# Kernel tuning notes

Hardware: AMD Instinct MI355X
Metric: run time of the kernel (lower is better)

Reference implementation:

```python
import jax, jax.numpy as jnp
import numpy as np

EPS = 1e-6  # torch F.pairwise_distance default eps (added to diff before norm)


def setup_inputs() -> dict:
    key = jax.random.key(0)
    k1, k2 = jax.random.split(key)
    B, D, n = 4096, 1024, 64
    K = n * n
    x = jax.random.normal(k1, (B, D), dtype=jnp.float32)
    weight = jax.random.normal(k2, (D, K), dtype=jnp.float32)  # SOM codebook
    # locations = [(gx, gy) for gx in range(n) for gy in range(n)]
    gx, gy = jnp.meshgrid(jnp.arange(n), jnp.arange(n), indexing='ij')
    locations = jnp.stack([gx, gy], axis=-1).reshape(K, 2).astype(jnp.float32)
    return {"x": x, "weight": weight, "locations": locations}


def _pairwise_l2(x, weight):
    # torch: norm(x[:, :, None] - weight[None] + EPS, p=2, dim=1) -> [B, K]
    # Expanded algebraically to avoid the [B, D, K] intermediate:
    D = x.shape[1]
    x2 = jnp.sum(x * x, axis=1, keepdims=True)            # [B, 1]
    w2 = jnp.sum(weight * weight, axis=0, keepdims=True)  # [1, K]
    xw = x @ weight                                        # [B, K] GEMM
    sx = jnp.sum(x, axis=1, keepdims=True)                 # [B, 1]
    sw = jnp.sum(weight, axis=0, keepdims=True)            # [1, K]
    d2 = x2 - 2.0 * xw + w2 + 2.0 * EPS * (sx - sw) + D * EPS * EPS
    return jnp.sqrt(jnp.maximum(d2, 0.0))


def reference(x, weight, locations):
    B = x.shape[0]
    dists = _pairwise_l2(x, weight)                        # [B, K]
    losses = jnp.min(dists, axis=1, keepdims=True)         # [B, 1]
    bmu_indexes = jnp.argmin(dists, axis=1, keepdims=True)  # [B, 1] int
    bmu_locations = locations[bmu_indexes]                 # [B, 1, 2]
    loss = jnp.sum(losses) / B                             # scalar
    return bmu_locations, loss, bmu_indexes
```

## Files before the change

kernel.cpp:

```cpp
#include <hip/hip_runtime.h>

#define EPS 1e-6f

constexpr int Bn = 4096;
constexpr int Dn = 1024;
constexpr int Kn = 4096;

typedef __attribute__((ext_vector_type(4))) float f32x4;
typedef __attribute__((ext_vector_type(2))) long long ll2;

__device__ inline int pk_fp8_lo(float a, float b, int old) {
    return __builtin_amdgcn_cvt_pk_fp8_f32(a, b, old, false);
}
__device__ inline int pk_fp8_hi(float a, float b, int old) {
    return __builtin_amdgcn_cvt_pk_fp8_f32(a, b, old, true);
}

__device__ inline float packcand(float s, int k) {
    unsigned b = __float_as_uint(fmaxf(s, 0.5f));
    return __uint_as_float((b & 0xFFFFF000u) | (unsigned)k);
}

__global__ __launch_bounds__(256) void som_prep(
    const float* __restrict__ x, const float* __restrict__ w,
    unsigned char* __restrict__ xf8, float* __restrict__ rrow,
    float* __restrict__ wtf, unsigned char* __restrict__ wf8,
    float* __restrict__ cpart, unsigned* __restrict__ ticket) {
    __shared__ float t[64][65];
    __shared__ float cp[4][64];
    __shared__ float red[8];
    const int tid = threadIdx.x;
    const int bid = blockIdx.x;
    if (bid == 0 && tid == 32) *ticket = 0u;
    if (bid < 2048) {
        const int lane = tid & 63, wid = tid >> 6;
        size_t i = (size_t)bid * 256 + tid;
        const float4* p = (const float4*)x;
        float4 a = p[i * 2], b = p[i * 2 + 1];
        int lo = pk_fp8_lo(a.x, a.y, 0); lo = pk_fp8_hi(a.z, a.w, lo);
        int hi = pk_fp8_lo(b.x, b.y, 0); hi = pk_fp8_hi(b.z, b.w, hi);
        ((int2*)xf8)[i] = make_int2(lo, hi);
        float s2 = a.x*a.x + a.y*a.y + a.z*a.z + a.w*a.w
                 + b.x*b.x + b.y*b.y + b.z*b.z + b.w*b.w;
        float s1 = a.x + a.y + a.z + a.w + b.x + b.y + b.z + b.w;
        #pragma unroll
        for (int off = 1; off < 64; off <<= 1) {
            s2 += __shfl_xor(s2, off);
            s1 += __shfl_xor(s1, off);
        }
        if (lane == 0) { red[wid] = s2; red[4 + wid] = s1; }
        __syncthreads();
        if (tid == 0)
            rrow[bid * 2] = (red[0] + red[1])
                + 2.f * EPS * (red[4] + red[5]) + (float)Dn * EPS * EPS;
        if (tid == 128)
            rrow[bid * 2 + 1] = (red[2] + red[3])
                + 2.f * EPS * (red[6] + red[7]) + (float)Dn * EPS * EPS;
    } else {
        const int tb = bid - 2048;
        const int kb = tb & 63, db = tb >> 6;
        const int k0 = kb * 64, d0 = db * 64;
        const int tx = tid & 63, ty = tid >> 6;
        #pragma unroll
        for (int i = 0; i < 16; ++i) {
            int d = i * 4 + ty;
            t[d][tx] = w[(size_t)(d0 + d) * Kn + k0 + tx];
        }
        __syncthreads();
        #pragma unroll
        for (int i = 0; i < 16; ++i) {
            int kr = i * 4 + ty;
            float v = t[tx][kr];
            wtf[(size_t)(k0 + kr) * Dn + d0 + tx] = v;
            wf8[(size_t)(k0 + kr) * Dn + d0 + tx] =
                (unsigned char)(pk_fp8_lo(v, v, 0) & 0xFF);
        }
        float cs = 0.f;
        #pragma unroll
        for (int j = 0; j < 16; ++j) {
            float v = t[ty * 16 + j][tx];
            cs = fmaf(v, v - 2.f * EPS, cs);
        }
        cp[ty][tx] = cs;
        __syncthreads();
        if (ty == 0)
            cpart[(size_t)db * Kn + k0 + tx] = cp[0][tx] + cp[1][tx] + cp[2][tx] + cp[3][tx];
    }
}

__global__ __launch_bounds__(256, 3) void som_gemm_fp8(
    const unsigned char* __restrict__ xf8, const unsigned char* __restrict__ wf8,
    const float* __restrict__ cpart, float* __restrict__ pval) {
    __shared__ __align__(16) unsigned char As[128 * 144];
    __shared__ __align__(16) unsigned char Bs[128 * 144];
    const int tid = threadIdx.x;
    const int lane = tid & 63;
    const int wid = tid >> 6;
    const int wm = wid >> 1, wn = wid & 1;
    const int f = blockIdx.x;
    const int xcd = f & 7;
    const int ib = f >> 3;
    const int rb = xcd * 4 + (ib & 3);
    const int cb = ib >> 2;
    const int rowBase = rb * 128, colBase = cb * 128;

    int offA[4];
    const unsigned char* gsrcA[4];
    const unsigned char* gsrcB[4];
    #pragma unroll
    for (int i = 0; i < 4; ++i) {
        int g = i * 256 + tid;
        int r = g >> 3, s = g & 7;
        offA[i] = r * 144 + (2 * (s & 1)) * 32 + (s >> 1) * 8;
        gsrcA[i] = xf8 + (size_t)(rowBase + r) * Dn + s * 16;
        gsrcB[i] = wf8 + (size_t)(colBase + r) * Dn + s * 16;
    }

    f32x4 acc[4][4] = {};
    ll2 ra[4], rbv[4];
    #pragma unroll
    for (int i = 0; i < 4; ++i) {
        ra[i]  = *(const ll2*)(gsrcA[i]);
        rbv[i] = *(const ll2*)(gsrcB[i]);
    }

    const int mrA = (wm * 64 + (lane & 15)) * 144;
    const int nrB = (wn * 64 + (lane & 15)) * 144;
    const int qoff = (lane >> 4) * 32;

    for (int it = 0; it < 8; ++it) {
        #pragma unroll
        for (int i = 0; i < 4; ++i) {
            *(long long*)&As[offA[i]]      = ra[i][0];
            *(long long*)&As[offA[i] + 32] = ra[i][1];
            *(long long*)&Bs[offA[i]]      = rbv[i][0];
            *(long long*)&Bs[offA[i] + 32] = rbv[i][1];
        }
        __syncthreads();
        if (it < 7) {
            int d0 = (it + 1) * 128;
            #pragma unroll
            for (int i = 0; i < 4; ++i) {
                ra[i]  = *(const ll2*)(gsrcA[i] + d0);
                rbv[i] = *(const ll2*)(gsrcB[i] + d0);
            }
        }
        #pragma unroll
        for (int kk2 = 0; kk2 < 2; ++kk2) {
            ll2 a2[4], b2[4];
            #pragma unroll
            for (int i = 0; i < 4; ++i) {
                a2[i] = *(const ll2*)&As[mrA + i * 16 * 144 + qoff + kk2 * 16];
                b2[i] = *(const ll2*)&Bs[nrB + i * 16 * 144 + qoff + kk2 * 16];
            }
            #pragma unroll
            for (int i = 0; i < 4; ++i)
                #pragma unroll
                for (int j = 0; j < 4; ++j) {
                    acc[i][j] = __builtin_amdgcn_mfma_f32_16x16x32_fp8_fp8(
                        a2[i][0], b2[j][0], acc[i][j], 0, 0, 0);
                    acc[i][j] = __builtin_amdgcn_mfma_f32_16x16x32_fp8_fp8(
                        a2[i][1], b2[j][1], acc[i][j], 0, 0, 0);
                }
        }
        __syncthreads();
    }

    const int cn = lane & 15, q = lane >> 4;
    const int nbase = colBase + wn * 64;
    float cv[4];
    #pragma unroll
    for (int j = 0; j < 4; ++j) {
        float s = 0.f;
        #pragma unroll
        for (int db = 0; db < 16; ++db)
            s += cpart[(size_t)db * Kn + nbase + j * 16 + cn];
        cv[j] = s;
    }
    #pragma unroll
    for (int i = 0; i < 4; ++i) {
        #pragma unroll
        for (int rg = 0; rg < 4; ++rg) {
            float p1 = 3.4e38f, p2 = 3.4e38f;
            #pragma unroll
            for (int j = 0; j < 4; ++j) {
                float p = packcand(fmaf(-2.f, acc[i][j][rg], cv[j]),
                                   nbase + j * 16 + cn);
                float lo = fminf(p1, p), hi = fmaxf(p1, p);
                p1 = lo; p2 = fminf(p2, hi);
            }
            #pragma unroll
            for (int off = 1; off < 16; off <<= 1) {
                float o1 = __shfl_xor(p1, off);
                float o2 = __shfl_xor(p2, off);
                float lo = fminf(p1, o1), hi = fmaxf(p1, o1);
                p1 = lo; p2 = fminf(hi, fminf(p2, o2));
            }
            if (cn == 0) {
                int mrow = rowBase + wm * 64 + i * 16 + q * 4 + rg;
                size_t e = (size_t)mrow * 128 + cb * 4 + wn * 2;
                pval[e] = p1; pval[e + 1] = p2;
            }
        }
    }
}

__global__ __launch_bounds__(256) void som_finalize(
    const float* __restrict__ x, const float* __restrict__ wtf,
    const float* __restrict__ cpart, const float* __restrict__ loc,
    const float* __restrict__ pval, const float* __restrict__ rrow,
    float* __restrict__ dist, float* __restrict__ out,
    unsigned* __restrict__ ticket) {
    __shared__ unsigned short lists[4][128];
    __shared__ float red2[4];
    __shared__ int finflag;
    const int tid = threadIdx.x;
    const int wv = tid >> 6, lane = tid & 63;
    const int row = blockIdx.x * 4 + wv;

    const float4* xr = (const float4*)(x + (size_t)row * Dn);
    float4 xv[4];
    #pragma unroll
    for (int j = 0; j < 4; ++j) xv[j] = xr[lane * 4 + j];
    const float rrv = rrow[row];

    float v0 = pval[(size_t)row * 128 + lane];
    float v1 = pval[(size_t)row * 128 + 64 + lane];
    float g = fminf(v0, v1);
    #pragma unroll
    for (int off = 1; off < 64; off <<= 1) g = fminf(g, __shfl_xor(g, off));
    const float thr = g + 30.0f;
    const unsigned long long m0 = __ballot(v0 <= thr);
    const unsigned long long m1 = __ballot(v1 <= thr);
    const int c0 = __popcll(m0);
    const int cnt = c0 + __popcll(m1);
    const unsigned long long below = (1ull << lane) - 1;
    if (v0 <= thr)
        lists[wv][__popcll(m0 & below)] =
            (unsigned short)(__float_as_uint(v0) & 0xFFF);
    if (v1 <= thr)
        lists[wv][c0 + __popcll(m1 & below)] =
            (unsigned short)(__float_as_uint(v1) & 0xFFF);

    float bestd2 = 3.4e38f; int bestk = 0x7fffffff;
    for (int i = 0; i < cnt; i += 2) {
        const int ka = lists[wv][i];
        const int kb = lists[wv][(i + 1 < cnt) ? i + 1 : i];
        const float4* wra = (const float4*)(wtf + (size_t)ka * Dn);
        const float4* wrb = (const float4*)(wtf + (size_t)kb * Dn);
        float pa = (lane < 16) ? cpart[(size_t)lane * Kn + ka] : 0.f;
        float pb = (lane < 16) ? cpart[(size_t)lane * Kn + kb] : 0.f;
        float da = 0.f, db = 0.f;
        #pragma unroll
        for (int j = 0; j < 4; ++j) {
            float4 wa = wra[lane * 4 + j];
            float4 wb = wrb[lane * 4 + j];
            da += xv[j].x * wa.x + xv[j].y * wa.y + xv[j].z * wa.z + xv[j].w * wa.w;
            db += xv[j].x * wb.x + xv[j].y * wb.y + xv[j].z * wb.z + xv[j].w * wb.w;
        }
        pa -= 2.f * da;
        pb -= 2.f * db;
        #pragma unroll
        for (int off = 1; off < 64; off <<= 1) {
            pa += __shfl_xor(pa, off);
            pb += __shfl_xor(pb, off);
        }
        const float d2a = rrv + pa, d2b = rrv + pb;
        if (d2a < bestd2 || (d2a == bestd2 && ka < bestk)) { bestd2 = d2a; bestk = ka; }
        if (i + 1 < cnt && (d2b < bestd2 || (d2b == bestd2 && kb < bestk))) {
            bestd2 = d2b; bestk = kb;
        }
    }
    if (lane == 0) {
        out[2 * row]     = loc[2 * bestk];
        out[2 * row + 1] = loc[2 * bestk + 1];
        out[8193 + row]  = (float)bestk;
        __hip_atomic_store(&dist[row], sqrtf(fmaxf(bestd2, 0.f)),
                           __ATOMIC_RELAXED, __HIP_MEMORY_SCOPE_AGENT);
    }
    __syncthreads();
    if (tid == 0) {
        unsigned t = __hip_atomic_fetch_add(ticket, 1u, __ATOMIC_ACQ_REL,
                                            __HIP_MEMORY_SCOPE_AGENT);
        finflag = (t == (unsigned)gridDim.x - 1u);
    }
    __syncthreads();
    if (finflag) {
        const int wid = tid >> 6;
        float s = 0.f;
        #pragma unroll
        for (int j = 0; j < 4; ++j) {
            int base = (tid + j * 256) * 4;
            float d0 = __hip_atomic_load(&dist[base + 0], __ATOMIC_RELAXED, __HIP_MEMORY_SCOPE_AGENT);
            float d1 = __hip_atomic_load(&dist[base + 1], __ATOMIC_RELAXED, __HIP_MEMORY_SCOPE_AGENT);
            float d2 = __hip_atomic_load(&dist[base + 2], __ATOMIC_RELAXED, __HIP_MEMORY_SCOPE_AGENT);
            float d3 = __hip_atomic_load(&dist[base + 3], __ATOMIC_RELAXED, __HIP_MEMORY_SCOPE_AGENT);
            s += ((d0 + d1) + d2) + d3;
        }
        #pragma unroll
        for (int off = 1; off < 64; off <<= 1) s += __shfl_xor(s, off);
        if (lane == 0) red2[wid] = s;
        __syncthreads();
        if (tid == 0)
            out[8192] = (red2[0] + red2[1] + red2[2] + red2[3]) * (1.0f / (float)Bn);
    }
}

extern "C" void kernel_launch(void* const* d_in, const int* in_sizes, int n_in,
                              void* d_out, int out_size, void* d_ws, size_t ws_size,
                              hipStream_t stream) {
    const float* x   = (const float*)d_in[0];
    const float* w   = (const float*)d_in[1];
    const float* loc = (const float*)d_in[2];
    float* out = (float*)d_out;

    float* rrow = (float*)d_ws;
    float* wtf  = rrow + Bn;
    unsigned char* wf8 = (unsigned char*)(wtf + (size_t)Kn * Dn);
    unsigned char* xf8 = wf8 + (size_t)Kn * Dn;
    float* pval = (float*)(xf8 + (size_t)Bn * Dn);
    float* cpart = pval + (size_t)Bn * 128;
    float* dist  = cpart + 16 * Kn;
    unsigned* ticket = (unsigned*)(dist + Bn);

    som_prep<<<3072, 256, 0, stream>>>(x, w, xf8, rrow, wtf, wf8, cpart, ticket);
    som_gemm_fp8<<<1024, 256, 0, stream>>>(xf8, wf8, cpart, pval);
    som_finalize<<<Bn / 4, 256, 0, stream>>>(x, wtf, cpart, loc, pval, rrow, dist, out, ticket);
}
```

Before: 160.3 us.

## Vectorize weight transpose stores and walk candidate ballots without shared lists

The weight transpose/quantize pass now loads and stores float4 rows and packs four FP8 values into one 32-bit store, replacing scalar per-element accesses and single-byte writes. The finalize kernel drops the shared-memory candidate list and iterates the ballot masks directly, broadcasting each candidate index with a shuffle and rescoring one candidate at a time instead of two. This is meant to cut memory transactions in prep and shared-memory traffic in finalize. It gives up the two-candidate interleaving that overlapped loads, and the new transpose read pattern may cause LDS bank conflicts.

```diff
diff --git a/kernel.cpp b/kernel.cpp
--- a/kernel.cpp
+++ b/kernel.cpp
@@ -60,21 +60,27 @@
         const int tb = bid - 2048;
         const int kb = tb & 63, db = tb >> 6;
         const int k0 = kb * 64, d0 = db * 64;
+        const int l16 = tid & 15, g16 = tid >> 4;
+        #pragma unroll
+        for (int i = 0; i < 4; ++i) {
+            int r = i * 16 + g16;
+            float4 v = *(const float4*)&w[(size_t)(d0 + r) * Kn + k0 + l16 * 4];
+            t[r][l16 * 4 + 0] = v.x; t[r][l16 * 4 + 1] = v.y;
+            t[r][l16 * 4 + 2] = v.z; t[r][l16 * 4 + 3] = v.w;
+        }
+        __syncthreads();
+        #pragma unroll
+        for (int i = 0; i < 4; ++i) {
+            int kr = i * 16 + g16;
+            float4 v;
+            v.x = t[l16 * 4 + 0][kr]; v.y = t[l16 * 4 + 1][kr];
+            v.z = t[l16 * 4 + 2][kr]; v.w = t[l16 * 4 + 3][kr];
+            *(float4*)&wtf[(size_t)(k0 + kr) * Dn + d0 + l16 * 4] = v;
+            int pk = pk_fp8_lo(v.x, v.y, 0); pk = pk_fp8_hi(v.z, v.w, pk);
+            *(unsigned int*)&wf8[(size_t)(k0 + kr) * Dn + d0 + l16 * 4] =
+                (unsigned int)pk;
+        }
         const int tx = tid & 63, ty = tid >> 6;
-        #pragma unroll
-        for (int i = 0; i < 16; ++i) {
-            int d = i * 4 + ty;
-            t[d][tx] = w[(size_t)(d0 + d) * Kn + k0 + tx];
-        }
-        __syncthreads();
-        #pragma unroll
-        for (int i = 0; i < 16; ++i) {
-            int kr = i * 4 + ty;
-            float v = t[tx][kr];
-            wtf[(size_t)(k0 + kr) * Dn + d0 + tx] = v;
-            wf8[(size_t)(k0 + kr) * Dn + d0 + tx] =
-                (unsigned char)(pk_fp8_lo(v, v, 0) & 0xFF);
-        }
         float cs = 0.f;
         #pragma unroll
         for (int j = 0; j < 16; ++j) {
@@ -211,12 +217,11 @@
     const float* __restrict__ pval, const float* __restrict__ rrow,
     float* __restrict__ dist, float* __restrict__ out,
     unsigned* __restrict__ ticket) {
-    __shared__ unsigned short lists[4][128];
     __shared__ float red2[4];
     __shared__ int finflag;
     const int tid = threadIdx.x;
-    const int wv = tid >> 6, lane = tid & 63;
-    const int row = blockIdx.x * 4 + wv;
+    const int lane = tid & 63;
+    const int row = blockIdx.x * 4 + (tid >> 6);
 
     const float4* xr = (const float4*)(x + (size_t)row * Dn);
     float4 xv[4];
@@ -230,45 +235,30 @@
     #pragma unroll
     for (int off = 1; off < 64; off <<= 1) g = fminf(g, __shfl_xor(g, off));
     const float thr = g + 30.0f;
-    const unsigned long long m0 = __ballot(v0 <= thr);
-    const unsigned long long m1 = __ballot(v1 <= thr);
-    const int c0 = __popcll(m0);
-    const int cnt = c0 + __popcll(m1);
-    const unsigned long long below = (1ull << lane) - 1;
-    if (v0 <= thr)
-        lists[wv][__popcll(m0 & below)] =
-            (unsigned short)(__float_as_uint(v0) & 0xFFF);
-    if (v1 <= thr)
-        lists[wv][c0 + __popcll(m1 & below)] =
-            (unsigned short)(__float_as_uint(v1) & 0xFFF);
+    unsigned long long m0 = __ballot(v0 <= thr);
+    unsigned long long m1 = __ballot(v1 <= thr);
 
     float bestd2 = 3.4e38f; int bestk = 0x7fffffff;
-    for (int i = 0; i < cnt; i += 2) {
-        const int ka = lists[wv][i];
-        const int kb = lists[wv][(i + 1 < cnt) ? i + 1 : i];
-        const float4* wra = (const float4*)(wtf + (size_t)ka * Dn);
-        const float4* wrb = (const float4*)(wtf + (size_t)kb * Dn);
-        float pa = (lane < 16) ? cpart[(size_t)lane * Kn + ka] : 0.f;
-        float pb = (lane < 16) ? cpart[(size_t)lane * Kn + kb] : 0.f;
-        float da = 0.f, db = 0.f;
-        #pragma unroll
-        for (int j = 0; j < 4; ++j) {
-            float4 wa = wra[lane * 4 + j];
-            float4 wb = wrb[lane * 4 + j];
-            da += xv[j].x * wa.x + xv[j].y * wa.y + xv[j].z * wa.z + xv[j].w * wa.w;
-            db += xv[j].x * wb.x + xv[j].y * wb.y + xv[j].z * wb.z + xv[j].w * wb.w;
-        }
-        pa -= 2.f * da;
-        pb -= 2.f * db;
-        #pragma unroll
-        for (int off = 1; off < 64; off <<= 1) {
-            pa += __shfl_xor(pa, off);
-            pb += __shfl_xor(pb, off);
-        }
-        const float d2a = rrv + pa, d2b = rrv + pb;
-        if (d2a < bestd2 || (d2a == bestd2 && ka < bestk)) { bestd2 = d2a; bestk = ka; }
-        if (i + 1 < cnt && (d2b < bestd2 || (d2b == bestd2 && kb < bestk))) {
-            bestd2 = d2b; bestk = kb;
+    #pragma unroll
+    for (int slot = 0; slot < 2; ++slot) {
+        unsigned long long m = slot ? m1 : m0;
+        float vs = slot ? v1 : v0;
+        while (m) {
+            int src = __builtin_ctzll(m); m &= m - 1;
+            int k = ((int)__float_as_uint(__shfl(vs, src))) & 0xFFF;
+            const float4* wr = (const float4*)(wtf + (size_t)k * Dn);
+            float pa = (lane < 16) ? cpart[(size_t)lane * Kn + k] : 0.f;
+            float da = 0.f;
+            #pragma unroll
+            for (int j = 0; j < 4; ++j) {
+                float4 wv = wr[lane * 4 + j];
+                da += xv[j].x * wv.x + xv[j].y * wv.y + xv[j].z * wv.z + xv[j].w * wv.w;
+            }
+            pa -= 2.f * da;
+            #pragma unroll
+            for (int off = 1; off < 64; off <<= 1) pa += __shfl_xor(pa, off);
+            float d2 = rrv + pa;
+            if (d2 < bestd2 || (d2 == bestd2 && k < bestk)) { bestd2 = d2; bestk = k; }
         }
     }
     if (lane == 0) {
```

New measurement: 157.0 us. -2.1%, faster.
